# Kernel optimization log

Measured on AMD Instinct MI355X. Metric: run time of the kernel, lower is better.

## Reference

```python
import jax, jax.numpy as jnp
import numpy as np

D_MODEL = 512
NUM_HEADS = 8
D_K = D_MODEL // NUM_HEADS


def setup_inputs() -> dict:
    key = jax.random.key(0)
    k0, k1, k2, k3, k4 = jax.random.split(key, 5)
    s = 1.0 / np.sqrt(D_MODEL)
    return {
        "x": jax.random.normal(k0, (2, 4096, D_MODEL), dtype=jnp.float32),
        "W_q": jax.random.normal(k1, (D_MODEL, D_MODEL), dtype=jnp.float32) * s,
        "W_k": jax.random.normal(k2, (D_MODEL, D_MODEL), dtype=jnp.float32) * s,
        "W_v": jax.random.normal(k3, (D_MODEL, D_MODEL), dtype=jnp.float32) * s,
        "W_o": jax.random.normal(k4, (D_MODEL, D_MODEL), dtype=jnp.float32) * s,
    }


def reference(x, W_q, W_k, W_v, W_o):
    B, S, _ = x.shape
    # project and split heads: (B, H, S, d_k)
    def split(t):
        return t.reshape(B, S, NUM_HEADS, D_K).transpose(0, 2, 1, 3)
    Q = split(x @ W_q)
    K = split(x @ W_k)
    V = split(x @ W_v)
    scale = jnp.sqrt(jnp.asarray(D_K, dtype=x.dtype))
    logits = jnp.einsum('bhqd,bhkd->bhqk', Q, K) / scale
    attn = jax.nn.softmax(logits, axis=-1)  # dropout is identity at inference
    out = jnp.einsum('bhqk,bhkd->bhqd', attn, V)
    concat = out.transpose(0, 2, 1, 3).reshape(B, S, D_MODEL)
    return concat @ W_o
```

## Files before the change

### kernel.cpp

```cpp
#include <hip/hip_runtime.h>
#include <hip/hip_bf16.h>


#define DMODEL 512
#define SEQ    4096
#define NTOK   8192
#define LDQK   1024

using f32x4 = __attribute__((ext_vector_type(4))) float;
using s16x8 = __attribute__((ext_vector_type(8))) short;
using u16x8 = __attribute__((ext_vector_type(8))) unsigned short;

static __device__ __forceinline__ unsigned short f2bf(float f) {
  union { float f; unsigned u; } v; v.f = f;
  unsigned r = v.u + 0x7fff + ((v.u >> 16) & 1);
  return (unsigned short)(r >> 16);
}

static __device__ __forceinline__ unsigned pack_bf2(float lo, float hi) {
  __hip_bfloat162 t = __float22bfloat162_rn(make_float2(lo, hi));
  union { __hip_bfloat162 b; unsigned u; } c; c.b = t; return c.u;
}

static __device__ __forceinline__ void gll16(const void* g, void* l) {
  __builtin_amdgcn_global_load_lds(
      (const __attribute__((address_space(1))) unsigned int*)g,
      (__attribute__((address_space(3))) unsigned int*)l, 16, 0, 0);
}

__global__ void prep_kernel(const float* __restrict__ x,
                            const float* __restrict__ Wq,
                            const float* __restrict__ Wk,
                            const float* __restrict__ Wv,
                            const float* __restrict__ Wo,
                            unsigned short* __restrict__ xb,
                            unsigned short* __restrict__ Wall, float c2) {
  __shared__ float T[64][65];
  const int bx = blockIdx.x;
  if (bx < 1024) {
    for (int i = bx * 256 + threadIdx.x; i < NTOK * DMODEL / 4; i += 262144) {
      float4 v = ((const float4*)x)[i];
      ushort4 o;
      o.x = f2bf(v.x); o.y = f2bf(v.y); o.z = f2bf(v.z); o.w = f2bf(v.w);
      ((ushort4*)xb)[i] = o;
    }
    return;
  }
  const int t = bx - 1024;
  const int y = t >> 6, sub = t & 63;
  const float* W = (y == 0) ? Wq : (y == 1) ? Wk : (y == 2) ? Wv : Wo;
  const float scale = (y == 0) ? c2 : 1.0f;
  const int tk = (sub & 7) * 64;
  const int tn = (sub >> 3) * 64;
  const int r  = threadIdx.x >> 2;
  const int cq = threadIdx.x & 3;
#pragma unroll
  for (int i = 0; i < 4; ++i) {
    int c = (cq + 4 * i) * 4;
    float4 v = *(const float4*)&W[(size_t)(tk + r) * 512 + tn + c];
    T[r][c + 0] = v.x * scale; T[r][c + 1] = v.y * scale;
    T[r][c + 2] = v.z * scale; T[r][c + 3] = v.w * scale;
  }
  __syncthreads();
  const int n  = threadIdx.x >> 2;
  const int k0 = (threadIdx.x & 3) * 16;
#pragma unroll
  for (int j4 = 0; j4 < 4; ++j4) {
    ushort4 o;
    o.x = f2bf(T[k0 + j4 * 4 + 0][n]);
    o.y = f2bf(T[k0 + j4 * 4 + 1][n]);
    o.z = f2bf(T[k0 + j4 * 4 + 2][n]);
    o.w = f2bf(T[k0 + j4 * 4 + 3][n]);
    *(ushort4*)&Wall[(size_t)y * 262144 + (size_t)(tn + n) * 512 + tk + k0 + j4 * 4] = o;
  }
}

__global__ __launch_bounds__(256, 3) void gemm_qkv(
    const unsigned short* __restrict__ xb,
    const unsigned short* __restrict__ Wall,
    unsigned short* __restrict__ QKb,
    unsigned short* __restrict__ Vtb)
{
  __shared__ unsigned short As[128 * 32];
  __shared__ unsigned short Bs[128 * 32];
  const int by = blockIdx.y;
  const bool vmode = (by >= 8);
  const unsigned short* A  = vmode ? (Wall + 2 * 262144) : xb;
  const unsigned short* Bt = vmode ? xb : Wall;
  const size_t bm = vmode ? (size_t)(by - 8) * 128 : (size_t)blockIdx.x * 128;
  const size_t bn = vmode ? (size_t)blockIdx.x * 128 : (size_t)by * 128;
  const int tid  = threadIdx.x;
  const int wave = tid >> 6, lane = tid & 63;
  const int q4 = lane >> 4, ln = lane & 15;
  const int wm = (wave >> 1) * 64, wn = (wave & 1) * 64;
  f32x4 acc[4][4] = {};
  const int srow = wave * 16 + (lane >> 2);
  const int scol = (lane & 3) * 8;

  const unsigned short* Ag  = A  + (bm + srow)      * 512 + scol;
  const unsigned short* Ag2 = A  + (bm + 64 + srow) * 512 + scol;
  const unsigned short* Bg  = Bt + (bn + srow)      * 512 + scol;
  const unsigned short* Bg2 = Bt + (bn + 64 + srow) * 512 + scol;
  unsigned short* Ad  = As + wave * 512;
  unsigned short* Ad2 = As + 2048 + wave * 512;
  unsigned short* Bd  = Bs + wave * 512;
  unsigned short* Bd2 = Bs + 2048 + wave * 512;

  for (int kt = 0; kt < 512; kt += 32) {
    __syncthreads();
    gll16(Ag + kt,  Ad);
    gll16(Ag2 + kt, Ad2);
    gll16(Bg + kt,  Bd);
    gll16(Bg2 + kt, Bd2);
    __syncthreads();
    s16x8 af[4], bfr[4];
#pragma unroll
    for (int i = 0; i < 4; i++)
      af[i] = *(const s16x8*)(As + (wm + i * 16 + ln) * 32 + q4 * 8);
#pragma unroll
    for (int i = 0; i < 4; i++)
      bfr[i] = *(const s16x8*)(Bs + (wn + i * 16 + ln) * 32 + q4 * 8);
#pragma unroll
    for (int mi = 0; mi < 4; mi++)
#pragma unroll
      for (int ni = 0; ni < 4; ni++)
        acc[mi][ni] = __builtin_amdgcn_mfma_f32_16x16x32_bf16(
            af[mi], bfr[ni], acc[mi][ni], 0, 0, 0);
  }
#pragma unroll
  for (int mi = 0; mi < 4; mi++)
#pragma unroll
    for (int r = 0; r < 4; ++r) {
      size_t row = bm + wm + mi * 16 + q4 * 4 + r;
#pragma unroll
      for (int ni = 0; ni < 4; ni++) {
        size_t col = bn + wn + ni * 16 + ln;
        unsigned short hv = f2bf(acc[mi][ni][r]);
        if (!vmode) {
          QKb[row * 1024 + col] = hv;
        } else {
          int b = (int)(col >> 12), s = (int)(col & 4095);
          int sp = (s & ~63) | (s & 32) | (((s >> 2) & 3) << 3) |
                   (((s >> 4) & 1) << 2) | (s & 3);
          Vtb[(size_t)b * 2097152 + row * 4096 + sp] = hv;
        }
      }
    }
}

__global__ __launch_bounds__(256, 2) void attn_kernel(
    const unsigned short* __restrict__ QK,
    const unsigned short* __restrict__ Vt,
    unsigned short* __restrict__ Oc)
{
  const int bid = blockIdx.x + 32 * (blockIdx.y + 8 * blockIdx.z);
  const int lin = (bid & 7) * 64 + (bid >> 3);
  const int qt = lin & 31, bh = lin >> 5;
  const int h = bh & 7, b = bh >> 3;
  const int tid = threadIdx.x, wave = tid >> 6, lane = tid & 63;
  const int q4 = lane >> 4, ln = lane & 15;
  __shared__ unsigned short Ks[2][64 * 64];
  __shared__ unsigned short Vs[2][64 * 64];
  const size_t rowbase = (size_t)b * SEQ;
  const size_t qrow0   = (size_t)qt * 128 + wave * 32;
  const unsigned short* Kp  = QK + rowbase * LDQK + 512 + h * 64;
  const unsigned short* VTp = Vt + ((size_t)(b * 8 + h) * 64) * SEQ;

  s16x8 qf[2][2];
#pragma unroll
  for (int mf = 0; mf < 2; ++mf) {
    const unsigned short* q = QK + (rowbase + qrow0 + mf * 16 + ln) * LDQK + h * 64;
    qf[mf][0] = *(const s16x8*)(q + q4 * 8);
    qf[mf][1] = *(const s16x8*)(q + 32 + q4 * 8);
  }
  f32x4 o[2][4] = {};
  f32x4 ol[2]   = {};

  s16x8 onesf;
#pragma unroll
  for (int j = 0; j < 8; ++j) onesf[j] = (short)0x3F80;

  const int rswz = (ln & 7) << 4;

  const int rlo = lane >> 3;
  const int sb  = (((lane & 7) << 4)) ^ (rlo << 4);
  const char* kgb = (const char*)Kp  + (size_t)(wave * 16 + rlo) * 2048 + sb;
  const char* vgb = (const char*)VTp + (size_t)(wave * 16 + rlo) * 8192 + sb;

  auto stage = [&](int tt, int nb) {
    char* Kd = (char*)Ks[nb] + wave * 2048;
    char* Vd = (char*)Vs[nb] + wave * 2048;
    const char* kg = kgb + (size_t)tt * 131072;
    const char* vg = vgb + (size_t)tt * 128;
    gll16(kg,         Kd);
    gll16(kg + 16384, Kd + 1024);
    gll16(vg,         Vd);
    gll16(vg + 65536, Vd + 1024);
  };

  stage(0, 0);
  __syncthreads();

  const f32x4 fz = {0.f, 0.f, 0.f, 0.f};

  s16x8 vfp[2][4];
  s16x8 pfp[2][2];

  {
    const char* Kc = (const char*)Ks[0];
    const char* Vc = (const char*)Vs[0];
    stage(1, 1);
    f32x4 s4[2][4];
#pragma unroll
    for (int ni = 0; ni < 4; ni++) {
      const char* kb = Kc + (ni * 16 + ln) * 128;
      s16x8 kf0 = *(const s16x8*)(kb + ((q4 * 16)      ^ rswz));
      s16x8 kf1 = *(const s16x8*)(kb + ((q4 * 16 + 64) ^ rswz));
      __builtin_amdgcn_s_setprio(1);
#pragma unroll
      for (int mf = 0; mf < 2; ++mf) {
        f32x4 acc0 = __builtin_amdgcn_mfma_f32_16x16x32_bf16(kf0, qf[mf][0], fz, 0, 0, 0);
        s4[mf][ni] = __builtin_amdgcn_mfma_f32_16x16x32_bf16(kf1, qf[mf][1], acc0, 0, 0, 0);
      }
      __builtin_amdgcn_s_setprio(0);
    }
#pragma unroll
    for (int ks = 0; ks < 2; ++ks)
#pragma unroll
      for (int ni = 0; ni < 4; ni++)
        vfp[ks][ni] = *(const s16x8*)(Vc + (ni * 16 + ln) * 128 +
                                      ((ks * 64 + q4 * 16) ^ rswz));
#pragma unroll
    for (int mf = 0; mf < 2; ++mf) {
      float e[4][4];
#pragma unroll
      for (int ni = 0; ni < 4; ni++)
#pragma unroll
        for (int r = 0; r < 4; ++r)
          e[ni][r] = __builtin_amdgcn_exp2f(s4[mf][ni][r]);
#pragma unroll
      for (int ks = 0; ks < 2; ++ks) {
        union { s16x8 v; unsigned u[4]; } pu;
        pu.u[0] = pack_bf2(e[2 * ks][0],     e[2 * ks][1]);
        pu.u[1] = pack_bf2(e[2 * ks][2],     e[2 * ks][3]);
        pu.u[2] = pack_bf2(e[2 * ks + 1][0], e[2 * ks + 1][1]);
        pu.u[3] = pack_bf2(e[2 * ks + 1][2], e[2 * ks + 1][3]);
        pfp[mf][ks] = pu.v;
      }
    }
    __syncthreads();
  }

#pragma unroll 2
  for (int t = 1; t < 64; ++t) {
    const int cur = t & 1;
    const char* Kc = (const char*)Ks[cur];
    const char* Vc = (const char*)Vs[cur];

    if (t + 1 < 64) stage(t + 1, cur ^ 1);

    f32x4 s4[2][4];
#pragma unroll
    for (int ni = 0; ni < 4; ni++) {
      const char* kb = Kc + (ni * 16 + ln) * 128;
      s16x8 kf0 = *(const s16x8*)(kb + ((q4 * 16)      ^ rswz));
      s16x8 kf1 = *(const s16x8*)(kb + ((q4 * 16 + 64) ^ rswz));
      __builtin_amdgcn_s_setprio(1);
#pragma unroll
      for (int mf = 0; mf < 2; ++mf) {
        f32x4 acc0 = __builtin_amdgcn_mfma_f32_16x16x32_bf16(kf0, qf[mf][0], fz, 0, 0, 0);
        s4[mf][ni] = __builtin_amdgcn_mfma_f32_16x16x32_bf16(kf1, qf[mf][1], acc0, 0, 0, 0);
      }
      __builtin_amdgcn_s_setprio(0);
    }

#pragma unroll
    for (int ks = 0; ks < 2; ++ks)
#pragma unroll
      for (int ni = 0; ni < 4; ni++)
#pragma unroll
        for (int mf = 0; mf < 2; ++mf)
          o[mf][ni] = __builtin_amdgcn_mfma_f32_16x16x32_bf16(pfp[mf][ks], vfp[ks][ni], o[mf][ni], 0, 0, 0);
#pragma unroll
    for (int mf = 0; mf < 2; ++mf)
#pragma unroll
      for (int ks = 0; ks < 2; ++ks)
        ol[mf] = __builtin_amdgcn_mfma_f32_16x16x32_bf16(pfp[mf][ks], onesf, ol[mf], 0, 0, 0);

    s16x8 vfc[2][4];
#pragma unroll
    for (int ks = 0; ks < 2; ++ks)
#pragma unroll
      for (int ni = 0; ni < 4; ni++)
        vfc[ks][ni] = *(const s16x8*)(Vc + (ni * 16 + ln) * 128 +
                                      ((ks * 64 + q4 * 16) ^ rswz));

    s16x8 pfc[2][2];
#pragma unroll
    for (int mf = 0; mf < 2; ++mf) {
      float e[4][4];
#pragma unroll
      for (int ni = 0; ni < 4; ni++)
#pragma unroll
        for (int r = 0; r < 4; ++r)
          e[ni][r] = __builtin_amdgcn_exp2f(s4[mf][ni][r]);
#pragma unroll
      for (int ks = 0; ks < 2; ++ks) {
        union { s16x8 v; unsigned u[4]; } pu;
        pu.u[0] = pack_bf2(e[2 * ks][0],     e[2 * ks][1]);
        pu.u[1] = pack_bf2(e[2 * ks][2],     e[2 * ks][3]);
        pu.u[2] = pack_bf2(e[2 * ks + 1][0], e[2 * ks + 1][1]);
        pu.u[3] = pack_bf2(e[2 * ks + 1][2], e[2 * ks + 1][3]);
        pfc[mf][ks] = pu.v;
      }
    }

#pragma unroll
    for (int ks = 0; ks < 2; ++ks)
#pragma unroll
      for (int ni = 0; ni < 4; ni++)
        vfp[ks][ni] = vfc[ks][ni];
#pragma unroll
    for (int mf = 0; mf < 2; ++mf)
#pragma unroll
      for (int ks = 0; ks < 2; ++ks)
        pfp[mf][ks] = pfc[mf][ks];

    __syncthreads();
  }

  __builtin_amdgcn_s_setprio(1);
#pragma unroll
  for (int ks = 0; ks < 2; ++ks)
#pragma unroll
    for (int ni = 0; ni < 4; ni++)
#pragma unroll
      for (int mf = 0; mf < 2; ++mf)
        o[mf][ni] = __builtin_amdgcn_mfma_f32_16x16x32_bf16(pfp[mf][ks], vfp[ks][ni], o[mf][ni], 0, 0, 0);
#pragma unroll
  for (int mf = 0; mf < 2; ++mf)
#pragma unroll
    for (int ks = 0; ks < 2; ++ks)
      ol[mf] = __builtin_amdgcn_mfma_f32_16x16x32_bf16(pfp[mf][ks], onesf, ol[mf], 0, 0, 0);
  __builtin_amdgcn_s_setprio(0);

#pragma unroll
  for (int mf = 0; mf < 2; ++mf)
#pragma unroll
    for (int r = 0; r < 4; ++r) {
      const float nv = 1.0f / ol[mf][r];
      const size_t row = rowbase + qrow0 + mf * 16 + q4 * 4 + r;
#pragma unroll
      for (int ni = 0; ni < 4; ni++)
        Oc[row * 512 + h * 64 + ni * 16 + ln] = f2bf(o[mf][ni][r] * nv);
    }
}

__global__ __launch_bounds__(256, 3) void gemm_out(
    const unsigned short* __restrict__ A,
    const unsigned short* __restrict__ Bt,
    float* __restrict__ C)
{
  __shared__ unsigned short As[128 * 32];
  __shared__ unsigned short Bs[64 * 32];
  const int tid  = threadIdx.x;
  const int wave = tid >> 6, lane = tid & 63;
  const int q4 = lane >> 4, ln = lane & 15;
  const size_t bm = (size_t)blockIdx.x * 128;
  const size_t bn = (size_t)blockIdx.y * 64;
  const int wm = (wave >> 1) * 64, wn = (wave & 1) * 32;
  f32x4 acc[4][2] = {};
  const int srow = wave * 16 + (lane >> 2);
  const int scol = (lane & 3) * 8;

  const unsigned short* Ag  = A  + (bm + srow)      * 512 + scol;
  const unsigned short* Ag2 = A  + (bm + 64 + srow) * 512 + scol;
  const unsigned short* Bg  = Bt + (bn + srow)      * 512 + scol;
  unsigned short* Ad  = As + wave * 512;
  unsigned short* Ad2 = As + 2048 + wave * 512;
  unsigned short* Bd  = Bs + wave * 512;

  for (int kt = 0; kt < 512; kt += 32) {
    __syncthreads();
    gll16(Ag + kt,  Ad);
    gll16(Ag2 + kt, Ad2);
    gll16(Bg + kt,  Bd);
    __syncthreads();
    s16x8 af[4], bfr[2];
#pragma unroll
    for (int i = 0; i < 4; i++)
      af[i] = *(const s16x8*)(As + (wm + i * 16 + ln) * 32 + q4 * 8);
#pragma unroll
    for (int i = 0; i < 2; i++)
      bfr[i] = *(const s16x8*)(Bs + (wn + i * 16 + ln) * 32 + q4 * 8);
#pragma unroll
    for (int mi = 0; mi < 4; mi++)
#pragma unroll
      for (int ni = 0; ni < 2; ni++)
        acc[mi][ni] = __builtin_amdgcn_mfma_f32_16x16x32_bf16(
            af[mi], bfr[ni], acc[mi][ni], 0, 0, 0);
  }
#pragma unroll
  for (int mi = 0; mi < 4; mi++)
#pragma unroll
    for (int r = 0; r < 4; ++r) {
      size_t row = bm + wm + mi * 16 + q4 * 4 + r;
#pragma unroll
      for (int ni = 0; ni < 2; ni++)
        C[row * 512 + bn + wn + ni * 16 + ln] = acc[mi][ni][r];
    }
}

extern "C" void kernel_launch(void* const* d_in, const int* in_sizes, int n_in,
                              void* d_out, int out_size, void* d_ws, size_t ws_size,
                              hipStream_t stream) {
  const float* x  = (const float*)d_in[0];
  const float* Wq = (const float*)d_in[1];
  const float* Wk = (const float*)d_in[2];
  const float* Wv = (const float*)d_in[3];
  const float* Wo = (const float*)d_in[4];

  char* ws = (char*)d_ws;
  unsigned short* xb    = (unsigned short*)(ws);
  unsigned short* Wall  = (unsigned short*)(ws + 8388608);
  unsigned short* QKb   = (unsigned short*)(ws + 10485760);
  unsigned short* Vtb   = (unsigned short*)(ws + 27262976);
  unsigned short* Oc    = (unsigned short*)(ws + 35651584);

  const float C2 = 0.125f * 1.44269504088896f;

  hipLaunchKernelGGL(prep_kernel, dim3(1280), dim3(256), 0, stream,
                     x, Wq, Wk, Wv, Wo, xb, Wall, C2);
  hipLaunchKernelGGL(gemm_qkv, dim3(64, 12), dim3(256), 0, stream,
                     xb, Wall, QKb, Vtb);
  hipLaunchKernelGGL(attn_kernel, dim3(32, 8, 2), dim3(256), 0, stream,
                     QKb, Vtb, Oc);
  hipLaunchKernelGGL(gemm_out, dim3(64, 8), dim3(256), 0, stream,
                     Oc, Wall + 3 * 262144, (float*)d_out);
}
```

Before: 185.6 us.

## Triple-buffer K/V tiles with vmcnt waits and compute row sums with VALU

Moves the attention K/V shared-memory staging from double to triple buffering, prefetching two tiles ahead. Full __syncthreads are replaced with partial vmcnt waits plus a raw barrier, so the in-flight loads for the next tile are not drained each iteration. It also drops the extra MFMAs against a ones vector that computed softmax denominators. Those sums are now accumulated in fp32 on the VALU and reduced with cross-lane shuffles at the end. The cost is more LDS per block, which could limit occupancy, and the denominator now sums fp32 exponentials instead of bf16-rounded ones, with extra wrap-around loads on the last iterations.

```diff
diff --git a/kernel.cpp b/kernel.cpp
--- a/kernel.cpp
+++ b/kernel.cpp
@@ -159,8 +159,8 @@
   const int h = bh & 7, b = bh >> 3;
   const int tid = threadIdx.x, wave = tid >> 6, lane = tid & 63;
   const int q4 = lane >> 4, ln = lane & 15;
-  __shared__ unsigned short Ks[2][64 * 64];
-  __shared__ unsigned short Vs[2][64 * 64];
+  __shared__ unsigned short Ks[3][64 * 64];
+  __shared__ unsigned short Vs[3][64 * 64];
   const size_t rowbase = (size_t)b * SEQ;
   const size_t qrow0   = (size_t)qt * 128 + wave * 32;
   const unsigned short* Kp  = QK + rowbase * LDQK + 512 + h * 64;
@@ -174,11 +174,7 @@
     qf[mf][1] = *(const s16x8*)(q + 32 + q4 * 8);
   }
   f32x4 o[2][4] = {};
-  f32x4 ol[2]   = {};
-
-  s16x8 onesf;
-#pragma unroll
-  for (int j = 0; j < 8; ++j) onesf[j] = (short)0x3F80;
+  float lp[2] = {};
 
   const int rswz = (ln & 7) << 4;
 
@@ -199,7 +195,10 @@
   };
 
   stage(0, 0);
-  __syncthreads();
+  stage(1, 1);
+  asm volatile("s_waitcnt vmcnt(4)" ::: "memory");
+  __builtin_amdgcn_s_barrier();
+  __builtin_amdgcn_sched_barrier(0);
 
   const f32x4 fz = {0.f, 0.f, 0.f, 0.f};
 
@@ -209,7 +208,7 @@
   {
     const char* Kc = (const char*)Ks[0];
     const char* Vc = (const char*)Vs[0];
-    stage(1, 1);
+    stage(2, 2);
     f32x4 s4[2][4];
 #pragma unroll
     for (int ni = 0; ni < 4; ni++) {
@@ -238,6 +237,11 @@
 #pragma unroll
         for (int r = 0; r < 4; ++r)
           e[ni][r] = __builtin_amdgcn_exp2f(s4[mf][ni][r]);
+      float t0 = (e[0][0] + e[0][1]) + (e[0][2] + e[0][3]);
+      float t1 = (e[1][0] + e[1][1]) + (e[1][2] + e[1][3]);
+      float t2 = (e[2][0] + e[2][1]) + (e[2][2] + e[2][3]);
+      float t3 = (e[3][0] + e[3][1]) + (e[3][2] + e[3][3]);
+      lp[mf] += (t0 + t1) + (t2 + t3);
 #pragma unroll
       for (int ks = 0; ks < 2; ++ks) {
         union { s16x8 v; unsigned u[4]; } pu;
@@ -248,16 +252,18 @@
         pfp[mf][ks] = pu.v;
       }
     }
-    __syncthreads();
-  }
-
+    asm volatile("s_waitcnt vmcnt(4)" ::: "memory");
+    __builtin_amdgcn_s_barrier();
+    __builtin_amdgcn_sched_barrier(0);
+  }
+
+  int bcur = 1, nbuf = 0;
 #pragma unroll 2
   for (int t = 1; t < 64; ++t) {
-    const int cur = t & 1;
-    const char* Kc = (const char*)Ks[cur];
-    const char* Vc = (const char*)Vs[cur];
-
-    if (t + 1 < 64) stage(t + 1, cur ^ 1);
+    const char* Kc = (const char*)Ks[bcur];
+    const char* Vc = (const char*)Vs[bcur];
+
+    stage((t + 2) & 63, nbuf);
 
     f32x4 s4[2][4];
 #pragma unroll
@@ -281,11 +287,6 @@
 #pragma unroll
         for (int mf = 0; mf < 2; ++mf)
           o[mf][ni] = __builtin_amdgcn_mfma_f32_16x16x32_bf16(pfp[mf][ks], vfp[ks][ni], o[mf][ni], 0, 0, 0);
-#pragma unroll
-    for (int mf = 0; mf < 2; ++mf)
-#pragma unroll
-      for (int ks = 0; ks < 2; ++ks)
-        ol[mf] = __builtin_amdgcn_mfma_f32_16x16x32_bf16(pfp[mf][ks], onesf, ol[mf], 0, 0, 0);
 
     s16x8 vfc[2][4];
 #pragma unroll
@@ -304,6 +305,11 @@
 #pragma unroll
         for (int r = 0; r < 4; ++r)
           e[ni][r] = __builtin_amdgcn_exp2f(s4[mf][ni][r]);
+      float t0 = (e[0][0] + e[0][1]) + (e[0][2] + e[0][3]);
+      float t1 = (e[1][0] + e[1][1]) + (e[1][2] + e[1][3]);
+      float t2 = (e[2][0] + e[2][1]) + (e[2][2] + e[2][3]);
+      float t3 = (e[3][0] + e[3][1]) + (e[3][2] + e[3][3]);
+      lp[mf] += (t0 + t1) + (t2 + t3);
 #pragma unroll
       for (int ks = 0; ks < 2; ++ks) {
         union { s16x8 v; unsigned u[4]; } pu;
@@ -326,7 +332,12 @@
       for (int ks = 0; ks < 2; ++ks)
         pfp[mf][ks] = pfc[mf][ks];
 
-    __syncthreads();
+    asm volatile("s_waitcnt vmcnt(4)" ::: "memory");
+    __builtin_amdgcn_s_barrier();
+    __builtin_amdgcn_sched_barrier(0);
+
+    bcur = (bcur == 2) ? 0 : bcur + 1;
+    nbuf = (nbuf == 2) ? 0 : nbuf + 1;
   }
 
   __builtin_amdgcn_s_setprio(1);
@@ -337,23 +348,23 @@
 #pragma unroll
       for (int mf = 0; mf < 2; ++mf)
         o[mf][ni] = __builtin_amdgcn_mfma_f32_16x16x32_bf16(pfp[mf][ks], vfp[ks][ni], o[mf][ni], 0, 0, 0);
-#pragma unroll
-  for (int mf = 0; mf < 2; ++mf)
-#pragma unroll
-    for (int ks = 0; ks < 2; ++ks)
-      ol[mf] = __builtin_amdgcn_mfma_f32_16x16x32_bf16(pfp[mf][ks], onesf, ol[mf], 0, 0, 0);
   __builtin_amdgcn_s_setprio(0);
 
 #pragma unroll
-  for (int mf = 0; mf < 2; ++mf)
+  for (int mf = 0; mf < 2; ++mf) {
+    float l = lp[mf];
+    l += __shfl_xor(l, 16, 64);
+    l += __shfl_xor(l, 32, 64);
+    const float inv = 1.0f / l;
 #pragma unroll
     for (int r = 0; r < 4; ++r) {
-      const float nv = 1.0f / ol[mf][r];
+      const float nv = __shfl(inv, q4 * 4 + r, 64);
       const size_t row = rowbase + qrow0 + mf * 16 + q4 * 4 + r;
 #pragma unroll
       for (int ni = 0; ni < 4; ni++)
         Oc[row * 512 + h * 64 + ni * 16 + ln] = f2bf(o[mf][ni][r] * nv);
     }
+  }
 }
 
 __global__ __launch_bounds__(256, 3) void gemm_out(
```

New measurement: 193.9 us. +4.5%, slower.
